# Optimization experiments

Measured on AMD Instinct MI355X. Metric: run time of the kernel, lower is better.

## Reference

```python
import jax, jax.numpy as jnp
import numpy as np

N_PTS = 20000  # points per cloud


def setup_inputs() -> dict:
    key = jax.random.key(0)
    k1, k2 = jax.random.split(key)
    preds = jax.random.normal(k1, (N_PTS, 3), dtype=jnp.float32)
    gts = jax.random.normal(k2, (1, N_PTS, 3), dtype=jnp.float32)
    return {"preds": preds, "gts": gts}


def reference(preds, gts):
    # x = gts: [B, Nx, 3]; y = preds.unsqueeze(0): [1, Ny, 3] (B must be 1 for bmm)
    y = preds[None]                                   # [1, Ny, 3]
    x = gts                                           # [1, Nx, 3]
    xx = jnp.sum(x * x, axis=-1)                      # [1, Nx]  (diag of x x^T)
    yy = jnp.sum(y * y, axis=-1)                      # [1, Ny]
    zz = jnp.einsum('bnd,bmd->bnm', x, y)             # [1, Nx, Ny]
    P = xx[:, :, None] + yy[:, None, :] - 2.0 * zz    # [1, Nx, Ny] squared dists
    dist1 = jnp.min(P, axis=1)                        # [1, Ny] min over gts points
    dist2 = jnp.min(P, axis=2)                        # [1, Nx] min over pred points
    idx1 = jnp.argmin(P, axis=1)                      # [1, Ny]
    idx2 = jnp.argmin(P, axis=2)                      # [1, Nx]
    return dist1, dist2, idx1, idx2
```

## Files before the change

kernel.cpp:

```cpp
#include <hip/hip_runtime.h>

#define N_PTS  20000
#define NG     128
#define NC     (NG * NG)
#define GMIN   (-6.0f)
#define GINV   (NG / 12.0f)
#define MARGIN 5e-4f
#define SSTRIDE (N_PTS / 64)
#define QB79   79

__device__ __forceinline__ float np_self_dot(float x, float y, float z) {
    return __fadd_rn(__fadd_rn(__fmul_rn(x, x), __fmul_rn(y, y)),
                     __fmul_rn(z, z));
}
__device__ __forceinline__ unsigned ordmap(float f) {
    unsigned b = __float_as_uint(f);
    return (b & 0x80000000u) ? ~b : (b | 0x80000000u);
}
__device__ __forceinline__ float invord(unsigned h) {
    return __uint_as_float((h & 0x80000000u) ? (h ^ 0x80000000u) : ~h);
}
__device__ __forceinline__ int cellC(float v) {
    int c = (int)((v - GMIN) * GINV);
    return c < 0 ? 0 : (c > NG - 1 ? NG - 1 : c);
}
__device__ __forceinline__ unsigned long long wave_min_u64(unsigned long long k) {
    #pragma unroll
    for (int m = 1; m < 64; m <<= 1) {
        unsigned long long o = __shfl_xor(k, m, 64);
        k = (o < k) ? o : k;
    }
    return k;
}
__device__ __forceinline__ int imin2(int a, int b) { return a < b ? a : b; }

__global__ __launch_bounds__(256) void k_hist(
    const float* __restrict__ preds, const float* __restrict__ gts,
    int* __restrict__ cursor)
{
    int t = blockIdx.x * 256 + threadIdx.x;
    if (t >= 2 * N_PTS) return;
    int cl = t / N_PTS, i = t - cl * N_PTS;
    const float* src = cl ? gts : preds;
    int cell = cellC(src[i*3+0]) * NG + cellC(src[i*3+1]);
    atomicAdd(&cursor[cl * NC + cell], 1);
}

__global__ __launch_bounds__(1024) void k_scan(
    int* __restrict__ cursor, int* __restrict__ bstart)
{
    __shared__ int psum[1024];
    int cl = blockIdx.x, t = threadIdx.x;

    int base = t * 16;
    int v[16], s = 0;
    #pragma unroll
    for (int i = 0; i < 16; ++i) { v[i] = cursor[cl * NC + base + i]; s += v[i]; }
    psum[t] = s;
    __syncthreads();
    for (int off = 1; off < 1024; off <<= 1) {
        int a = (t >= off) ? psum[t - off] : 0;
        __syncthreads();
        psum[t] += a;
        __syncthreads();
    }
    int run = psum[t] - s;
    #pragma unroll
    for (int i = 0; i < 16; ++i) {
        bstart[cl * (NC + 1) + base + i] = run;
        cursor[cl * NC + base + i] = run;
        run += v[i];
    }
    if (t == 1023) bstart[cl * (NC + 1) + NC] = run;
}

__global__ __launch_bounds__(256) void k_scatter(
    const float* __restrict__ preds, const float* __restrict__ gts,
    int* __restrict__ cursor, float4* __restrict__ sorted)
{
    int t = blockIdx.x * 256 + threadIdx.x;
    if (t >= 2 * N_PTS) return;
    int cl = t / N_PTS, i = t - cl * N_PTS;
    const float* src = cl ? gts : preds;
    float x = src[i*3+0], y = src[i*3+1], z = src[i*3+2];
    int cell = cellC(x) * NG + cellC(y);
    int pos = atomicAdd(&cursor[cl * NC + cell], 1);
    sorted[(size_t)cl * N_PTS + pos] = make_float4(x, y, z, __int_as_float(i));
}

__global__ __launch_bounds__(64) void k_main(
    const float4* __restrict__ sorted, const int* __restrict__ bstart,
    float* __restrict__ out)
{
    int wid  = blockIdx.x;
    int lane = threadIdx.x;
    int dir  = wid / N_PTS;
    int qpos = wid - dir * N_PTS;
    int rcl  = 1 - dir;

    const float4* rs = sorted + (size_t)rcl * N_PTS;
    const int*    cs = bstart + rcl * (NC + 1);

    float4 qv    = sorted[(size_t)dir * N_PTS + qpos];
    int    origq = __float_as_int(qv.w);
    float qx = qv.x, qy = qv.y, qz = qv.z;
    float sq = np_self_dot(qx, qy, qz);

    unsigned long long key = ~0ULL;

#define EVAL(r)                                                            \
    {   float sr = np_self_dot((r).x, (r).y, (r).z);                       \
        float zz = __fadd_rn(__fadd_rn(__fmul_rn(qx, (r).x),               \
                                       __fmul_rn(qy, (r).y)),              \
                             __fmul_rn(qz, (r).z));                        \
        float P  = __fsub_rn(__fadd_rn(sq, sr), __fadd_rn(zz, zz));        \
        unsigned long long kk =                                            \
            ((unsigned long long)ordmap(P) << 32) | __float_as_uint((r).w);\
        key = (kk < key) ? kk : key; }

#define SCAN_BOX(xL, xR, yL, yR)                                           \
    for (int x0 = (xL); x0 <= (xR); x0 += 32) {                            \
        int nrows = imin2((xR) - x0 + 1, 32);                              \
        int xr  = imin2(x0 + (lane & 31), (xR));                           \
        int col = (lane < 32) ? (yL) : ((yR) + 1);                         \
        int bnd = cs[xr * NG + col];                                       \
        for (int rr = 0; rr < nrows; ++rr) {                               \
            int lo = __shfl(bnd, rr, 64);                                  \
            int hi = __shfl(bnd, 32 + rr, 64);                             \
            int p = lo + lane;                                             \
            for (; p + 64 < hi; p += 128) {                                \
                float4 r0 = rs[p];                                         \
                float4 r1 = rs[p + 64];             \
                EVAL(r0) EVAL(r1)                                          \
            }                                                              \
            if (p < hi) { float4 r0 = rs[p]; EVAL(r0) }                    \
        }                                                                  \
    }

    float4 samp = rs[lane * SSTRIDE];

    int cx = cellC(qx), cy = cellC(qy);
    int sxL = cx > 0 ? cx - 1 : 0, sxR = cx < NG-1 ? cx + 1 : NG-1;
    int syL = cy > 0 ? cy - 1 : 0, syR = cy < NG-1 ? cy + 1 : NG-1;
    SCAN_BOX(sxL, sxR, syL, syR)
    EVAL(samp)

    key = wave_min_u64(key);
    float W = sqrtf(invord((unsigned)(key >> 32)) + MARGIN);
    int txL = cellC(qx - W), txR = cellC(qx + W);
    int tyL = cellC(qy - W), tyR = cellC(qy + W);
    if (!(txL >= sxL && txR <= sxR && tyL >= syL && tyR <= syR)) {
        SCAN_BOX(txL, txR, tyL, tyR)
        key = wave_min_u64(key);
    }
#undef SCAN_BOX
#undef EVAL

    if (lane == 0) {
        out[dir * N_PTS + origq]       = invord((unsigned)(key >> 32));
        out[(2 + dir) * N_PTS + origq] = (float)(unsigned)(key & 0xFFFFFFFFu);
    }
}

__device__ __forceinline__ float np_pair(float sq, float sr,
                                         float qx, float qy, float qz,
                                         float rx, float ry, float rz) {
    float zz = __fadd_rn(__fadd_rn(__fmul_rn(qx, rx), __fmul_rn(qy, ry)),
                         __fmul_rn(qz, rz));
    return __fsub_rn(__fadd_rn(sq, sr), __fadd_rn(zz, zz));
}

__global__ __launch_bounds__(256) void chamfer_direct_kernel(
    const float* __restrict__ preds, const float* __restrict__ gts,
    float* __restrict__ out)
{
    __shared__ float4 spts[256];
    int bid = blockIdx.x;
    int dir = bid / QB79;
    int qb  = bid - dir * QB79;
    int q   = qb * 256 + threadIdx.x;

    const float* qpts = (dir == 0) ? preds : gts;
    const float* rpts = (dir == 0) ? gts   : preds;

    int qc = (q < N_PTS) ? q : (N_PTS - 1);
    float qx = qpts[qc*3+0], qy = qpts[qc*3+1], qz = qpts[qc*3+2];
    float sq = np_self_dot(qx, qy, qz);
    float best = 3.4e38f;
    int   bidx = 0;

    for (int t = 0; t < N_PTS; t += 256) {
        int cnt = min(256, N_PTS - t);
        __syncthreads();
        if ((int)threadIdx.x < cnt) {
            int j = t + threadIdx.x;
            float rx = rpts[j*3+0], ry = rpts[j*3+1], rz = rpts[j*3+2];
            spts[threadIdx.x] = make_float4(rx, ry, rz, np_self_dot(rx, ry, rz));
        }
        __syncthreads();
        for (int k = 0; k < cnt; ++k) {
            float4 r = spts[k];
            float d = np_pair(sq, r.w, qx, qy, qz, r.x, r.y, r.z);
            if (d < best) { best = d; bidx = t + k; }
        }
    }
    if (q < N_PTS) {
        out[dir * N_PTS + q]       = best;
        out[(2 + dir) * N_PTS + q] = (float)bidx;
    }
}

extern "C" void kernel_launch(void* const* d_in, const int* in_sizes, int n_in,
                              void* d_out, int out_size, void* d_ws, size_t ws_size,
                              hipStream_t stream) {
    const float* preds = (const float*)d_in[0];
    const float* gts   = (const float*)d_in[1];
    float* out = (float*)d_out;

    char* w = (char*)d_ws;
    size_t sorted_b = (size_t)2 * N_PTS * sizeof(float4);
    size_t bstart_b = (size_t)2 * (NC + 1) * sizeof(int);
    size_t cursor_b = (size_t)2 * NC * sizeof(int);
    size_t need = sorted_b + bstart_b + cursor_b;

    if (ws_size >= need) {
        float4* sorted = (float4*)w;
        int* bstart = (int*)(w + sorted_b);
        int* cursor = (int*)(w + sorted_b + bstart_b);

        hipMemsetAsync(cursor, 0, cursor_b, stream);
        k_hist<<<(2 * N_PTS + 255) / 256, 256, 0, stream>>>(preds, gts, cursor);
        k_scan<<<2, 1024, 0, stream>>>(cursor, bstart);
        k_scatter<<<(2 * N_PTS + 255) / 256, 256, 0, stream>>>(
            preds, gts, cursor, sorted);
        k_main<<<2 * N_PTS, 64, 0, stream>>>(sorted, bstart, out);
    } else {
        chamfer_direct_kernel<<<2 * QB79, 256, 0, stream>>>(preds, gts, out);
    }
}
```

Measured before the change: 123.3 us.

## Stream contiguous cell ranges instead of per-row box scans; wave-shuffle scan

The nearest-neighbour search now reads one contiguous range of the row-major sorted buffer, from the first cell of the box to the last, instead of walking each x-row of the box separately. The refinement pass only extends that range at either end. This removes the per-row boundary lookups, shuffles and short inner loops, and unrolls the stream four-wide. The cost is that each range also covers every y-column between the box's rows, so many more candidate points get evaluated, especially in dense central cells. Separately, the prefix-scan kernel switches from a shared-memory Hillis-Steele scan to wave shuffles with vector loads, and the sample load is issued earlier.

```diff
diff --git a/kernel.cpp b/kernel.cpp
--- a/kernel.cpp
+++ b/kernel.cpp
@@ -32,7 +32,6 @@
     }
     return k;
 }
-__device__ __forceinline__ int imin2(int a, int b) { return a < b ? a : b; }
 
 __global__ __launch_bounds__(256) void k_hist(
     const float* __restrict__ preds, const float* __restrict__ gts,
@@ -49,26 +48,45 @@
 __global__ __launch_bounds__(1024) void k_scan(
     int* __restrict__ cursor, int* __restrict__ bstart)
 {
-    __shared__ int psum[1024];
+    __shared__ int wsum[16];
+    __shared__ int wpre[16];
     int cl = blockIdx.x, t = threadIdx.x;
-
-    int base = t * 16;
-    int v[16], s = 0;
-    #pragma unroll
-    for (int i = 0; i < 16; ++i) { v[i] = cursor[cl * NC + base + i]; s += v[i]; }
-    psum[t] = s;
+    int wave = t >> 6, lane = t & 63;
+
+    int base = cl * NC + t * 16;
+    const int4* c4 = (const int4*)(cursor + base);
+    int4 a = c4[0], b = c4[1], c = c4[2], d = c4[3];
+    int v[16] = { a.x, a.y, a.z, a.w, b.x, b.y, b.z, b.w,
+                  c.x, c.y, c.z, c.w, d.x, d.y, d.z, d.w };
+    int s = 0;
+    #pragma unroll
+    for (int i = 0; i < 16; ++i) s += v[i];
+
+    int ps = s;
+    #pragma unroll
+    for (int m = 1; m < 64; m <<= 1) {
+        int o = __shfl_up(ps, m, 64);
+        if (lane >= m) ps += o;
+    }
+    if (lane == 63) wsum[wave] = ps;
     __syncthreads();
-    for (int off = 1; off < 1024; off <<= 1) {
-        int a = (t >= off) ? psum[t - off] : 0;
-        __syncthreads();
-        psum[t] += a;
-        __syncthreads();
-    }
-    int run = psum[t] - s;
+    if (t < 16) {
+        int x = wsum[t];
+        int px = x;
+        #pragma unroll
+        for (int m = 1; m < 16; m <<= 1) {
+            int o = __shfl_up(px, m, 16);
+            if ((t & 15) >= m) px += o;
+        }
+        wpre[t] = px - x;
+    }
+    __syncthreads();
+
+    int run = wpre[wave] + (ps - s);
     #pragma unroll
     for (int i = 0; i < 16; ++i) {
-        bstart[cl * (NC + 1) + base + i] = run;
-        cursor[cl * NC + base + i] = run;
+        bstart[cl * (NC + 1) + t * 16 + i] = run;
+        cursor[base + i] = run;
         run += v[i];
     }
     if (t == 1023) bstart[cl * (NC + 1) + NC] = run;
@@ -101,7 +119,8 @@
     const float4* rs = sorted + (size_t)rcl * N_PTS;
     const int*    cs = bstart + rcl * (NC + 1);
 
-    float4 qv    = sorted[(size_t)dir * N_PTS + qpos];
+    float4 samp = rs[lane * SSTRIDE];
+    float4 qv   = sorted[(size_t)dir * N_PTS + qpos];
     int    origq = __float_as_int(qv.w);
     float qx = qv.x, qy = qv.y, qz = qv.z;
     float sq = np_self_dot(qx, qy, qz);
@@ -118,42 +137,38 @@
             ((unsigned long long)ordmap(P) << 32) | __float_as_uint((r).w);\
         key = (kk < key) ? kk : key; }
 
-#define SCAN_BOX(xL, xR, yL, yR)                                           \
-    for (int x0 = (xL); x0 <= (xR); x0 += 32) {                            \
-        int nrows = imin2((xR) - x0 + 1, 32);                              \
-        int xr  = imin2(x0 + (lane & 31), (xR));                           \
-        int col = (lane < 32) ? (yL) : ((yR) + 1);                         \
-        int bnd = cs[xr * NG + col];                                       \
-        for (int rr = 0; rr < nrows; ++rr) {                               \
-            int lo = __shfl(bnd, rr, 64);                                  \
-            int hi = __shfl(bnd, 32 + rr, 64);                             \
-            int p = lo + lane;                                             \
-            for (; p + 64 < hi; p += 128) {                                \
-                float4 r0 = rs[p];                                         \
-                float4 r1 = rs[p + 64];             \
-                EVAL(r0) EVAL(r1)                                          \
-            }                                                              \
-            if (p < hi) { float4 r0 = rs[p]; EVAL(r0) }                    \
+#define STREAM(LO, HI)                                                     \
+    {   int p = (LO) + lane;                                               \
+        for (; p + 192 < (HI); p += 256) {                                 \
+            float4 r0 = rs[p],       r1 = rs[p + 64];                      \
+            float4 r2 = rs[p + 128], r3 = rs[p + 192];                     \
+            EVAL(r0) EVAL(r1) EVAL(r2) EVAL(r3)                            \
         }                                                                  \
-    }
-
-    float4 samp = rs[lane * SSTRIDE];
+        for (; p + 64 < (HI); p += 128) {                                  \
+            float4 r0 = rs[p], r1 = rs[p + 64];                            \
+            EVAL(r0) EVAL(r1)                                              \
+        }                                                                  \
+        if (p < (HI)) { float4 r0 = rs[p]; EVAL(r0) }                      \
+    }
 
     int cx = cellC(qx), cy = cellC(qy);
     int sxL = cx > 0 ? cx - 1 : 0, sxR = cx < NG-1 ? cx + 1 : NG-1;
     int syL = cy > 0 ? cy - 1 : 0, syR = cy < NG-1 ? cy + 1 : NG-1;
-    SCAN_BOX(sxL, sxR, syL, syR)
+    int slo = cs[sxL * NG + syL];
+    int shi = cs[sxR * NG + syR + 1];
+    STREAM(slo, shi)
     EVAL(samp)
 
     key = wave_min_u64(key);
     float W = sqrtf(invord((unsigned)(key >> 32)) + MARGIN);
     int txL = cellC(qx - W), txR = cellC(qx + W);
     int tyL = cellC(qy - W), tyR = cellC(qy + W);
-    if (!(txL >= sxL && txR <= sxR && tyL >= syL && tyR <= syR)) {
-        SCAN_BOX(txL, txR, tyL, tyR)
-        key = wave_min_u64(key);
-    }
-#undef SCAN_BOX
+    int lo2 = cs[txL * NG + tyL];
+    int hi2 = cs[txR * NG + tyR + 1];
+    if (lo2 < slo) STREAM(lo2, slo)
+    if (hi2 > shi) STREAM(shi, hi2)
+    key = wave_min_u64(key);
+#undef STREAM
 #undef EVAL
 
     if (lane == 0) {
```

Result: slower. 126.6 us (+2.7%).
